# Kernel tuning notes

Measured on AMD Instinct MI355X. Metric: run time of the kernel, lower is better.

Reference implementation:

```python
import jax, jax.numpy as jnp
import numpy as np

D_MODEL = 768
N_LAYER = 4
VOCAB = 10000
N_MELS = 80
D_STATE = 16
D_CONV = 4
DT_RANK = 48          # ceil(768/16)
D_INNER = 1536        # expand * d_model
B_SZ, L_SEQ = 2, 1024


def rmsnorm(x, w, eps=1e-5):
    return x * jax.lax.rsqrt(jnp.mean(x * x, axis=-1, keepdims=True) + eps) * w


def causal_depthwise_conv(x, w, b):
    # x: (b, l, d_inner); w: (d_inner, 1, d_conv); torch Conv1d with padding=d_conv-1, truncated to l
    xc = jax.lax.conv_general_dilated(
        jnp.transpose(x, (0, 2, 1)), w, window_strides=(1,),
        padding=[(D_CONV - 1, 0)], dimension_numbers=('NCH', 'OIH', 'NCH'),
        feature_group_count=D_INNER)
    xc = xc + b[None, :, None]
    return jnp.transpose(xc, (0, 2, 1))


def selective_scan(u, dt, A, B, C, D):
    # u, dt: (b,l,d_in); A: (d_in,n); B,C: (b,l,n); D: (d_in,)
    dA = jnp.einsum('bld,dn->bldn', dt, A)
    dB_u = jnp.einsum('bld,bld,bln->bldn', dt, u, B)
    dA = jnp.clip(dA, -20, None)
    # shift dA by one step (exclusive cumulative decay), cumsum mode
    dA_shift = jnp.pad(dA[:, 1:], ((0, 0), (1, 0), (0, 0), (0, 0)))
    dA_cumsum = jnp.exp(jnp.cumsum(dA_shift, axis=1))
    x = jnp.cumsum(dB_u / (dA_cumsum + 1e-12), axis=1) * dA_cumsum
    y = jnp.einsum('bldn,bln->bld', x, C)
    return y + u * D


def mamba_block(x, rms_w, in_w, cw, cb, xp_w, dt_w, dt_b, A_log, Dp, out_w):
    h = rmsnorm(x, rms_w)
    xz = h @ in_w                       # (b,l,2*d_inner)
    xi, res = jnp.split(xz, 2, axis=-1)
    xi = jax.nn.silu(causal_depthwise_conv(xi, cw, cb))
    A = -jnp.exp(A_log.astype(jnp.float32))
    x_dbl = xi @ xp_w                   # (b,l,dt_rank+2n)
    delta = x_dbl[..., :DT_RANK]
    Bm = x_dbl[..., DT_RANK:DT_RANK + D_STATE]
    Cm = x_dbl[..., DT_RANK + D_STATE:]
    delta = jax.nn.softplus(delta @ dt_w + dt_b)
    y = selective_scan(xi, delta, A, Bm, Cm, Dp.astype(jnp.float32))
    y = y * jax.nn.silu(res)
    return y @ out_w + x


def setup_inputs():
    key = jax.random.key(0)
    ks = jax.random.split(key, 8)
    s = 0.02
    return {
        'input_ids': jax.random.randint(ks[0], (B_SZ, L_SEQ), 0, VOCAB),
        'embedding': jax.random.normal(ks[1], (VOCAB, D_MODEL), jnp.float32) * s,
        'rms_w': jnp.ones((N_LAYER, D_MODEL), jnp.float32),
        'in_proj_w': jax.random.normal(ks[2], (N_LAYER, D_MODEL, 2 * D_INNER), jnp.float32) * s,
        'conv_w': jax.random.normal(ks[3], (N_LAYER, D_INNER, 1, D_CONV), jnp.float32) * 0.1,
        'conv_b': jnp.zeros((N_LAYER, D_INNER), jnp.float32),
        'x_proj_w': jax.random.normal(ks[4], (N_LAYER, D_INNER, DT_RANK + 2 * D_STATE), jnp.float32) * s,
        'dt_proj_w': jax.random.normal(ks[5], (N_LAYER, DT_RANK, D_INNER), jnp.float32) * s,
        'dt_proj_b': jnp.zeros((N_LAYER, D_INNER), jnp.float32),
        'A_log': jnp.broadcast_to(jnp.log(jnp.arange(1, D_STATE + 1, dtype=jnp.float32)), (N_LAYER, D_INNER, D_STATE)) + 0.0,
        'D_param': jnp.ones((N_LAYER, D_INNER), jnp.float32),
        'out_proj_w': jax.random.normal(ks[6], (N_LAYER, D_INNER, D_MODEL), jnp.float32) * s,
        'norm_f_w': jnp.ones((D_MODEL,), jnp.float32),
        'head_w': jax.random.normal(ks[7], (D_MODEL, N_MELS), jnp.float32) * s,
    }


def reference(input_ids, embedding, rms_w, in_proj_w, conv_w, conv_b, x_proj_w,
              dt_proj_w, dt_proj_b, A_log, D_param, out_proj_w, norm_f_w, head_w):
    x = embedding[input_ids]            # (b,l,d)
    for i in range(N_LAYER):
        x = mamba_block(x, rms_w[i], in_proj_w[i], conv_w[i], conv_b[i],
                        x_proj_w[i], dt_proj_w[i], dt_proj_b[i], A_log[i],
                        D_param[i], out_proj_w[i])
    x = rmsnorm(x, norm_f_w)
    return x @ head_w                   # (b,l,n_mels)
```

## Files before the change

kernel.cpp:

```cpp
#include <hip/hip_runtime.h>
#include <hip/hip_bf16.h>
#include <math.h>

#define D_MODEL 768
#define N_LAYER 4
#define D_STATE 16
#define D_CONV  4
#define DT_RANK 48
#define D_INNER 1536
#define B_SZ    2
#define L_SEQ   1024
#define N_MELS  80
#define ROWS    (B_SZ * L_SEQ)

typedef __bf16 bf16x8 __attribute__((ext_vector_type(8)));
typedef unsigned short u16x8 __attribute__((ext_vector_type(8)));
typedef float  f32x4  __attribute__((ext_vector_type(4)));

__device__ __forceinline__ float fast_exp2(float x) {
    float r; asm("v_exp_f32 %0, %1" : "=v"(r) : "v"(x)); return r;
}
__device__ __forceinline__ float fast_exp(float x) {
    return fast_exp2(x * 1.44269504f);
}
__device__ __forceinline__ float fast_rcp(float x) {
    float r; asm("v_rcp_f32 %0, %1" : "=v"(r) : "v"(x)); return r;
}
__device__ __forceinline__ float silu_f(float v) {
    return v * fast_rcp(1.0f + fast_exp(-v));
}
__device__ __forceinline__ float softplus_f(float v) {
    return fmaxf(v, 0.0f) + log1pf(expf(-fabsf(v)));
}
__device__ __forceinline__ unsigned short f2bf(float f) {
    unsigned int u = __float_as_uint(f);
    unsigned int r = (u + 0x7FFFu + ((u >> 16) & 1u)) >> 16;
    return (unsigned short)r;
}
__device__ __forceinline__ float bf2f(unsigned short v) {
    return __uint_as_float(((unsigned int)v) << 16);
}

__global__ void embed_head_kernel(const int* __restrict__ ids,
                                  const float* __restrict__ emb,
                                  float* __restrict__ x,
                                  const float* __restrict__ head_w,
                                  unsigned short* __restrict__ headT) {
    int i = blockIdx.x * 256 + threadIdx.x;
    if (i < ROWS * D_MODEL) {
        int r = i / D_MODEL, c = i - r * D_MODEL;
        x[i] = emb[(size_t)ids[r] * D_MODEL + c];
    } else {
        int j = i - ROWS * D_MODEL;
        if (j < N_MELS * D_MODEL) {
            int c = j / D_MODEL, r = j - c * D_MODEL;
            headT[j] = f2bf(head_w[(size_t)r * N_MELS + c]);
        }
    }
}

__global__ void rmsnorm_kernel(const float* __restrict__ x,
                               const float* __restrict__ w,
                               unsigned short* __restrict__ hb) {
    int row = blockIdx.x;
    const float* xr = x + (size_t)row * D_MODEL;
    int tid = threadIdx.x;
    float p = 0.f;
    for (int c = tid; c < D_MODEL; c += 256) { float v = xr[c]; p = fmaf(v, v, p); }
    for (int off = 32; off >= 1; off >>= 1) p += __shfl_down(p, off, 64);
    __shared__ float ws[4];
    int lane = tid & 63, wv = tid >> 6;
    if (lane == 0) ws[wv] = p;
    __syncthreads();
    if (tid == 0) ws[0] = ws[0] + ws[1] + ws[2] + ws[3];
    __syncthreads();
    float scale = 1.0f / sqrtf(ws[0] / (float)D_MODEL + 1e-5f);
    for (int c = tid; c < D_MODEL; c += 256)
        hb[(size_t)row * D_MODEL + c] = f2bf(xr[c] * scale * w[c]);
}

__global__ void prep_weights_kernel(const float* __restrict__ in_wi,
                                    const float* __restrict__ out_wi,
                                    const float* __restrict__ xp_wi,
                                    const float* __restrict__ dt_wi,
                                    unsigned short* __restrict__ wt_in,
                                    unsigned short* __restrict__ wt_out,
                                    unsigned short* __restrict__ xpT,
                                    unsigned short* __restrict__ dtwT) {
    __shared__ float t[32][33];
    int bx = blockIdx.x;
    int tid = threadIdx.x;
    if (bx < 3456) {
        const float* src; unsigned short* dst; int R, C, cy, cx;
        if (bx < 2304) {
            src = in_wi; dst = wt_in; R = D_MODEL; C = 2 * D_INNER;
            cy = bx / 96; cx = bx - cy * 96;
        } else {
            int tt = bx - 2304;
            src = out_wi; dst = wt_out; R = D_INNER; C = D_MODEL;
            cy = tt / 24; cx = tt - cy * 24;
        }
        int tx = tid & 31, ty = tid >> 5;
        int r0 = cy * 32, c0 = cx * 32;
#pragma unroll
        for (int i = 0; i < 4; i++)
            t[ty + i * 8][tx] = src[(size_t)(r0 + ty + i * 8) * C + c0 + tx];
        __syncthreads();
#pragma unroll
        for (int i = 0; i < 4; i++)
            dst[(size_t)(c0 + ty + i * 8) * R + r0 + tx] = f2bf(t[tx][ty + i * 8]);
    } else {
        int i = (bx - 3456) * 256 + tid;
        if (i < 80 * D_INNER) {
            int c = i / D_INNER, r = i - c * D_INNER;
            xpT[i] = f2bf(xp_wi[(size_t)r * 80 + c]);
        } else {
            int i2 = i - 80 * D_INNER;
            int c = i2 >> 6, r = i2 & 63;
            dtwT[i2] = (r < DT_RANK) ? f2bf(dt_wi[(size_t)r * D_INNER + c])
                                     : (unsigned short)0;
        }
    }
}

__global__ void reduce_cvt_kernel(const float* __restrict__ part,
                                  float* __restrict__ xdbl,
                                  unsigned short* __restrict__ xdblb,
                                  int nsplit) {
    int i = blockIdx.x * 256 + threadIdx.x;
    if (i >= ROWS * 80) return;
    float s = 0.f;
    for (int k = 0; k < nsplit; k++) s += part[(size_t)k * ROWS * 80 + i];
    xdbl[i] = s;
    int r = i / 80, c = i - r * 80;
    if (c < DT_RANK) xdblb[r * 64 + c] = f2bf(s);
    else if (c >= 64) xdblb[r * 64 + c - 16] = 0;
}

__global__ void reduce_split_kernel(const float* __restrict__ part,
                                    float* __restrict__ dst,
                                    int MN, int nsplit) {
    int i = blockIdx.x * 256 + threadIdx.x;
    if (i >= MN) return;
    float s = 0.f;
    for (int k = 0; k < nsplit; k++) s += part[(size_t)k * MN + i];
    dst[i] = s;
}

__global__ __launch_bounds__(256) void mfma_gemm64(
        const unsigned short* __restrict__ A,
        const unsigned short* __restrict__ BT,
        const float* __restrict__ bias, const float* __restrict__ resid,
        float* __restrict__ Cf, unsigned short* __restrict__ Cb,
        int M, int N, int K, int ldc, int act, int bias_mode) {
    __shared__ unsigned short As[64][72];
    __shared__ unsigned short Bs[128][72];
    int tid = threadIdx.x;
    int row0 = blockIdx.y * 64, col0 = blockIdx.x * 128;
    int wave = tid >> 6, lane = tid & 63;
    int wr = (wave >> 1) * 32, wc = (wave & 1) * 64;
    int lm = lane & 15, lq = lane >> 4;
    int sr = tid >> 3, seg = tid & 7;
    const unsigned short* Ap0 = A  + (size_t)(row0 + sr) * K + seg * 8;
    const unsigned short* Ap1 = A  + (size_t)(row0 + 32 + sr) * K + seg * 8;
    const unsigned short* Bp0 = BT + (size_t)(col0 + sr) * K + seg * 8;
    const unsigned short* Bp1 = BT + (size_t)(col0 + 32 + sr) * K + seg * 8;
    const unsigned short* Bp2 = BT + (size_t)(col0 + 64 + sr) * K + seg * 8;
    const unsigned short* Bp3 = BT + (size_t)(col0 + 96 + sr) * K + seg * 8;
    f32x4 acc[2][4] = {};
    bf16x8 pa0 = *(const bf16x8*)Ap0;
    bf16x8 pa1 = *(const bf16x8*)Ap1;
    bf16x8 pb0 = *(const bf16x8*)Bp0;
    bf16x8 pb1 = *(const bf16x8*)Bp1;
    bf16x8 pb2 = *(const bf16x8*)Bp2;
    bf16x8 pb3 = *(const bf16x8*)Bp3;
    *(bf16x8*)&As[sr][seg * 8]      = pa0;
    *(bf16x8*)&As[32 + sr][seg * 8] = pa1;
    *(bf16x8*)&Bs[sr][seg * 8]      = pb0;
    *(bf16x8*)&Bs[32 + sr][seg * 8] = pb1;
    *(bf16x8*)&Bs[64 + sr][seg * 8] = pb2;
    *(bf16x8*)&Bs[96 + sr][seg * 8] = pb3;
    for (int k0 = 0; k0 < K; k0 += 64) {
        __syncthreads();
        bool more = (k0 + 64 < K);
        if (more) {
            pa0 = *(const bf16x8*)(Ap0 + k0 + 64);
            pa1 = *(const bf16x8*)(Ap1 + k0 + 64);
            pb0 = *(const bf16x8*)(Bp0 + k0 + 64);
            pb1 = *(const bf16x8*)(Bp1 + k0 + 64);
            pb2 = *(const bf16x8*)(Bp2 + k0 + 64);
            pb3 = *(const bf16x8*)(Bp3 + k0 + 64);
        }
#pragma unroll
        for (int ks = 0; ks < 2; ks++) {
            bf16x8 af[2], bfr[4];
#pragma unroll
            for (int i = 0; i < 2; i++)
                af[i] = *(const bf16x8*)&As[wr + i * 16 + lm][ks * 32 + lq * 8];
#pragma unroll
            for (int j = 0; j < 4; j++)
                bfr[j] = *(const bf16x8*)&Bs[wc + j * 16 + lm][ks * 32 + lq * 8];
#pragma unroll
            for (int i = 0; i < 2; i++)
#pragma unroll
                for (int j = 0; j < 4; j++)
                    acc[i][j] = __builtin_amdgcn_mfma_f32_16x16x32_bf16(af[i], bfr[j], acc[i][j], 0, 0, 0);
        }
        __syncthreads();
        if (more) {
            *(bf16x8*)&As[sr][seg * 8]      = pa0;
            *(bf16x8*)&As[32 + sr][seg * 8] = pa1;
            *(bf16x8*)&Bs[sr][seg * 8]      = pb0;
            *(bf16x8*)&Bs[32 + sr][seg * 8] = pb1;
            *(bf16x8*)&Bs[64 + sr][seg * 8] = pb2;
            *(bf16x8*)&Bs[96 + sr][seg * 8] = pb3;
        }
    }
#pragma unroll
    for (int i = 0; i < 2; i++) {
#pragma unroll
        for (int ii = 0; ii < 4; ii++) {
            int row = row0 + wr + i * 16 + lq * 4 + ii;
#pragma unroll
            for (int j = 0; j < 4; j++) {
                int col = col0 + wc + j * 16 + lm;
                float v = acc[i][j][ii];
                if (bias) v += bias[bias_mode ? row : col];
                if (act == 1) v = softplus_f(v);
                if (resid) v += resid[(size_t)row * ldc + col];
                if (Cf) Cf[(size_t)row * ldc + col] = v;
                else    Cb[(size_t)row * ldc + col] = f2bf(v);
            }
        }
    }
}

template<bool AT>
__global__ __launch_bounds__(256) void mfma_gemm32(
        const unsigned short* __restrict__ A,
        const unsigned short* __restrict__ BT,
        const float* __restrict__ bias, const float* __restrict__ resid,
        float* __restrict__ Cf, unsigned short* __restrict__ Cb,
        int M, int N, int K, int ldc, int act, int bias_mode) {
    __shared__ unsigned short As[32][72];
    __shared__ unsigned short Bs[128][72];
    int tid = threadIdx.x;
    int row0 = blockIdx.y * 32, col0 = blockIdx.x * 128;
    int wave = tid >> 6, lane = tid & 63;
    int wc = wave * 32;
    int lm = lane & 15, lq = lane >> 4;
    int sr = tid >> 3, seg = tid & 7;
    const unsigned short* Bp0 = BT + (size_t)(col0 + sr) * K + seg * 8;
    const unsigned short* Bp1 = BT + (size_t)(col0 + 32 + sr) * K + seg * 8;
    const unsigned short* Bp2 = BT + (size_t)(col0 + 64 + sr) * K + seg * 8;
    const unsigned short* Bp3 = BT + (size_t)(col0 + 96 + sr) * K + seg * 8;
    int akk = tid >> 2, arc = (tid & 3) * 8;
    const unsigned short* ApT = AT ? (A + (size_t)akk * M + row0 + arc) : nullptr;
    const unsigned short* Ap  = AT ? nullptr : (A + (size_t)(row0 + sr) * K + seg * 8);
    f32x4 acc[2][2] = {};
    u16x8 pa;
    if (AT) pa = *(const u16x8*)ApT;
    else    pa = *(const u16x8*)Ap;
    bf16x8 pb0 = *(const bf16x8*)Bp0;
    bf16x8 pb1 = *(const bf16x8*)Bp1;
    bf16x8 pb2 = *(const bf16x8*)Bp2;
    bf16x8 pb3 = *(const bf16x8*)Bp3;
    if (AT) {
#pragma unroll
        for (int j = 0; j < 8; j++) As[arc + j][akk] = pa[j];
    } else {
        *(u16x8*)&As[sr][seg * 8] = pa;
    }
    *(bf16x8*)&Bs[sr][seg * 8]      = pb0;
    *(bf16x8*)&Bs[32 + sr][seg * 8] = pb1;
    *(bf16x8*)&Bs[64 + sr][seg * 8] = pb2;
    *(bf16x8*)&Bs[96 + sr][seg * 8] = pb3;
    for (int k0 = 0; k0 < K; k0 += 64) {
        __syncthreads();
        bool more = (k0 + 64 < K);
        if (more) {
            if (AT) pa = *(const u16x8*)(ApT + (size_t)(k0 + 64) * M);
            else    pa = *(const u16x8*)(Ap + k0 + 64);
            pb0 = *(const bf16x8*)(Bp0 + k0 + 64);
            pb1 = *(const bf16x8*)(Bp1 + k0 + 64);
            pb2 = *(const bf16x8*)(Bp2 + k0 + 64);
            pb3 = *(const bf16x8*)(Bp3 + k0 + 64);
        }
#pragma unroll
        for (int ks = 0; ks < 2; ks++) {
            bf16x8 af[2], bfr[2];
#pragma unroll
            for (int i = 0; i < 2; i++)
                af[i] = *(const bf16x8*)&As[i * 16 + lm][ks * 32 + lq * 8];
#pragma unroll
            for (int j = 0; j < 2; j++)
                bfr[j] = *(const bf16x8*)&Bs[wc + j * 16 + lm][ks * 32 + lq * 8];
#pragma unroll
            for (int i = 0; i < 2; i++)
#pragma unroll
                for (int j = 0; j < 2; j++)
                    acc[i][j] = __builtin_amdgcn_mfma_f32_16x16x32_bf16(af[i], bfr[j], acc[i][j], 0, 0, 0);
        }
        __syncthreads();
        if (more) {
            if (AT) {
#pragma unroll
                for (int j = 0; j < 8; j++) As[arc + j][akk] = pa[j];
            } else {
                *(u16x8*)&As[sr][seg * 8] = pa;
            }
            *(bf16x8*)&Bs[sr][seg * 8]      = pb0;
            *(bf16x8*)&Bs[32 + sr][seg * 8] = pb1;
            *(bf16x8*)&Bs[64 + sr][seg * 8] = pb2;
            *(bf16x8*)&Bs[96 + sr][seg * 8] = pb3;
        }
    }
#pragma unroll
    for (int i = 0; i < 2; i++) {
#pragma unroll
        for (int ii = 0; ii < 4; ii++) {
            int row = row0 + i * 16 + lq * 4 + ii;
#pragma unroll
            for (int j = 0; j < 2; j++) {
                int col = col0 + wc + j * 16 + lm;
                float v = acc[i][j][ii];
                if (bias) v += bias[bias_mode ? row : col];
                if (act == 1) v = softplus_f(v);
                if (resid) v += resid[(size_t)row * ldc + col];
                if (Cf) Cf[(size_t)row * ldc + col] = v;
                else    Cb[(size_t)row * ldc + col] = f2bf(v);
            }
        }
    }
}

template<bool AT>
__global__ __launch_bounds__(256) void mfma_skinny(
        const unsigned short* __restrict__ A,
        const float* __restrict__ AfT,
        const unsigned short* __restrict__ BT,
        float* __restrict__ part,
        int M, int K, int kchunk) {
    constexpr int N = 80, NT = 5;
    __shared__ unsigned short As[128][40];
    __shared__ unsigned short Bs[80][40];
    int tid = threadIdx.x;
    int row0 = blockIdx.x * 128;
    int kb = blockIdx.y * kchunk, ke = kb + kchunk;
    float* myout = part + (size_t)blockIdx.y * M * N;
    int wave = tid >> 6, lane = tid & 63;
    int wr = wave * 32;
    int lm = lane & 15, lq = lane >> 4;
    int ar0 = tid >> 2, ar1 = (tid + 256) >> 2, aseg = tid & 3;
    const unsigned short* Ap0 = AT ? nullptr : (A + (size_t)(row0 + ar0) * K + aseg * 8);
    const unsigned short* Ap1 = AT ? nullptr : (A + (size_t)(row0 + ar1) * K + aseg * 8);
    int srl = tid >> 5, src4 = (tid & 31) * 4;
    const float* Af0 = AT ? (AfT + (size_t)(srl + 0) * M + row0 + src4) : nullptr;
    const float* Af1 = AT ? (AfT + (size_t)(srl + 8) * M + row0 + src4) : nullptr;
    const float* Af2 = AT ? (AfT + (size_t)(srl + 16) * M + row0 + src4) : nullptr;
    const float* Af3 = AT ? (AfT + (size_t)(srl + 24) * M + row0 + src4) : nullptr;
    const unsigned short* Bp0 = BT + (size_t)ar0 * K + aseg * 8;
    const unsigned short* Bp1 = BT + (size_t)ar1 * K + aseg * 8;
    bool haveB1 = (tid < 64);
    f32x4 acc[2][NT] = {};
    bf16x8 pa0, pa1;
    f32x4 qa0, qa1, qa2, qa3;
    if (AT) {
        qa0 = *(const f32x4*)(Af0 + (size_t)kb * M);
        qa1 = *(const f32x4*)(Af1 + (size_t)kb * M);
        qa2 = *(const f32x4*)(Af2 + (size_t)kb * M);
        qa3 = *(const f32x4*)(Af3 + (size_t)kb * M);
    } else {
        pa0 = *(const bf16x8*)(Ap0 + kb);
        pa1 = *(const bf16x8*)(Ap1 + kb);
    }
    bf16x8 pb0 = *(const bf16x8*)(Bp0 + kb);
    bf16x8 pb1 = {};
    if (haveB1) pb1 = *(const bf16x8*)(Bp1 + kb);
    if (AT) {
#pragma unroll
        for (int e = 0; e < 4; e++) {
            As[src4 + e][srl]      = f2bf(qa0[e]);
            As[src4 + e][srl + 8]  = f2bf(qa1[e]);
            As[src4 + e][srl + 16] = f2bf(qa2[e]);
            As[src4 + e][srl + 24] = f2bf(qa3[e]);
        }
    } else {
        *(bf16x8*)&As[ar0][aseg * 8] = pa0;
        *(bf16x8*)&As[ar1][aseg * 8] = pa1;
    }
    *(bf16x8*)&Bs[ar0][aseg * 8] = pb0;
    if (haveB1) *(bf16x8*)&Bs[ar1][aseg * 8] = pb1;
    for (int k0 = kb; k0 < ke; k0 += 32) {
        __syncthreads();
        bool more = (k0 + 32 < ke);
        if (more) {
            if (AT) {
                qa0 = *(const f32x4*)(Af0 + (size_t)(k0 + 32) * M);
                qa1 = *(const f32x4*)(Af1 + (size_t)(k0 + 32) * M);
                qa2 = *(const f32x4*)(Af2 + (size_t)(k0 + 32) * M);
                qa3 = *(const f32x4*)(Af3 + (size_t)(k0 + 32) * M);
            } else {
                pa0 = *(const bf16x8*)(Ap0 + k0 + 32);
                pa1 = *(const bf16x8*)(Ap1 + k0 + 32);
            }
            pb0 = *(const bf16x8*)(Bp0 + k0 + 32);
            if (haveB1) pb1 = *(const bf16x8*)(Bp1 + k0 + 32);
        }
        bf16x8 af[2], bfr[NT];
#pragma unroll
        for (int i = 0; i < 2; i++) af[i] = *(const bf16x8*)&As[wr + i * 16 + lm][lq * 8];
#pragma unroll
        for (int j = 0; j < NT; j++) bfr[j] = *(const bf16x8*)&Bs[j * 16 + lm][lq * 8];
#pragma unroll
        for (int i = 0; i < 2; i++)
#pragma unroll
            for (int j = 0; j < NT; j++)
                acc[i][j] = __builtin_amdgcn_mfma_f32_16x16x32_bf16(af[i], bfr[j], acc[i][j], 0, 0, 0);
        __syncthreads();
        if (more) {
            if (AT) {
#pragma unroll
                for (int e = 0; e < 4; e++) {
                    As[src4 + e][srl]      = f2bf(qa0[e]);
                    As[src4 + e][srl + 8]  = f2bf(qa1[e]);
                    As[src4 + e][srl + 16] = f2bf(qa2[e]);
                    As[src4 + e][srl + 24] = f2bf(qa3[e]);
                }
            } else {
                *(bf16x8*)&As[ar0][aseg * 8] = pa0;
                *(bf16x8*)&As[ar1][aseg * 8] = pa1;
            }
            *(bf16x8*)&Bs[ar0][aseg * 8] = pb0;
            if (haveB1) *(bf16x8*)&Bs[ar1][aseg * 8] = pb1;
        }
    }
#pragma unroll
    for (int i = 0; i < 2; i++) {
#pragma unroll
        for (int ii = 0; ii < 4; ii++) {
            int row = row0 + wr + i * 16 + lq * 4 + ii;
#pragma unroll
            for (int j = 0; j < NT; j++) {
                int col = j * 16 + lm;
                myout[(size_t)row * N + col] = acc[i][j][ii];
            }
        }
    }
}

__global__ __launch_bounds__(256) void conv_silu_kernel(
        const unsigned short* __restrict__ xzb,
        const float* __restrict__ cw,
        const float* __restrict__ cb,
        float* __restrict__ uT,
        unsigned short* __restrict__ resT) {
    __shared__ unsigned short s_xz[67][66];
    __shared__ float us[64][65];
    int tid = threadIdx.x;
    int d0 = blockIdx.x * 64, r0 = blockIdx.y * 64;
    bool atStart = (r0 & (L_SEQ - 1)) == 0;
    for (int idx = tid; idx < 67 * 64; idx += 256) {
        int rr = idx >> 6, cc2 = idx & 63;
        unsigned short v = 0;
        if (rr >= 3 || !atStart)
            v = xzb[(size_t)(r0 - 3 + rr) * (2 * D_INNER) + d0 + cc2];
        s_xz[rr][cc2] = v;
    }
    __syncthreads();
    int cc = tid & 63, ty = tid >> 6;
    const float* wp = cw + (size_t)(d0 + cc) * D_CONV;
    float w0 = wp[0], w1 = wp[1], w2 = wp[2], w3 = wp[3];
    float bb = cb[d0 + cc];
    for (int rr = ty; rr < 64; rr += 4) {
        float s = bb;
        s = fmaf(bf2f(s_xz[rr + 0][cc]), w0, s);
        s = fmaf(bf2f(s_xz[rr + 1][cc]), w1, s);
        s = fmaf(bf2f(s_xz[rr + 2][cc]), w2, s);
        s = fmaf(bf2f(s_xz[rr + 3][cc]), w3, s);
        us[rr][cc] = silu_f(s);
    }
    __syncthreads();
    int tx = tid & 63, dy = tid >> 6;
    for (int dd = dy; dd < 64; dd += 4)
        uT[(size_t)(d0 + dd) * ROWS + r0 + tx] = us[tx][dd];
    __syncthreads();
    for (int idx = tid; idx < 64 * 64; idx += 256) {
        int rr = idx >> 6, cc2 = idx & 63;
        s_xz[rr][cc2] = xzb[(size_t)(r0 + rr) * (2 * D_INNER) + D_INNER + d0 + cc2];
    }
    __syncthreads();
    for (int dd = dy; dd < 64; dd += 4)
        resT[(size_t)(d0 + dd) * ROWS + r0 + tx] = s_xz[tx][dd];
}

__global__ __launch_bounds__(256) void scan_kernel(
        const float* __restrict__ deltaT,
        const float* __restrict__ uT,
        const float* __restrict__ xdbl,
        const unsigned short* __restrict__ resT,
        const float* __restrict__ A_log,
        const float* __restrict__ Dp,
        unsigned short* __restrict__ ygT) {
    int tid = threadIdx.x;
    int n = tid & 15, c = tid >> 4;
    int bd = blockIdx.x;
    int b = bd / D_INNER, d = bd - b * D_INNER;
    int row0 = b * L_SEQ;
    float a2 = -fast_exp(A_log[d * D_STATE + n]) * 1.44269504f;
    float Dd = Dp[d];
    __shared__ float2 s_du[L_SEQ + 16];
    __shared__ float cs1[16][17];
    __shared__ float cs2[16][17];
    __shared__ float gmv[16];
    const float* dptr = deltaT + (size_t)d * ROWS + row0;
    const float* uptr = uT + (size_t)d * ROWS + row0;
    for (int e = tid; e < L_SEQ; e += 256)
        s_du[e + (e >> 6)] = make_float2(dptr[e], uptr[e]);
    __syncthreads();
    {
        int l0 = c * 64, sb = l0 + c;
        bool notfirst = (c != 0);
        float sum = 0.f;
#pragma unroll 8
        for (int j = 0; j < 64; j++) {
            float dA = fmaxf(s_du[sb + j].x * a2, -28.8539008f);
            if (j > 0 || notfirst) sum += dA;
        }
        cs1[n][c] = sum;
    }
    __syncthreads();
    float cbase = 0.f;
    for (int cc = 0; cc < c; cc++) cbase += cs1[n][cc];
    float gm = cbase;
    gm = fmaxf(gm, __shfl_xor(gm, 1, 16));
    gm = fmaxf(gm, __shfl_xor(gm, 2, 16));
    gm = fmaxf(gm, __shfl_xor(gm, 4, 16));
    gm = fmaxf(gm, __shfl_xor(gm, 8, 16));
    if (n == 0) gmv[c] = gm;
    __syncthreads();
    int lc = 16;
    for (int cc = 1; cc < 16; cc++)
        if (gmv[cc] <= -150.0f) { lc = cc; break; }
    int clen = lc * 4;
    int l0b = c * clen;
    int lend = lc * 64;
    {
        float sum = 0.f;
        for (int j = 0; j < clen; j++) {
            int l = l0b + j;
            float dA = fmaxf(s_du[l + (l >> 6)].x * a2, -28.8539008f);
            if (l > 0) sum += dA;
        }
        cs1[n][c] = sum;
    }
    __syncthreads();
    float cbase_b = 0.f;
    for (int cc = 0; cc < c; cc++) cbase_b += cs1[n][cc];
    const float* xBbase = xdbl + (size_t)row0 * 80 + DT_RANK + n;
    {
        float Cacc = cbase_b, psum = 0.f;
        for (int j = 0; j < clen; j++) {
            int l = l0b + j;
            float2 du = s_du[l + (l >> 6)];
            float dA = fmaxf(du.x * a2, -28.8539008f);
            if (l > 0) Cacc += dA;
            float S = fast_exp2(Cacc);
            float r = fast_rcp(S + 1e-12f);
            psum = fmaf(du.x * du.y * xBbase[l * 80], r, psum);
        }
        cs2[n][c] = psum;
    }
    __syncthreads();
    float pbase = 0.f;
    for (int cc = 0; cc < c; cc++) pbase += cs2[n][cc];
    {
        float Cacc = cbase_b, P = pbase;
        for (int j = 0; j < clen; j++) {
            int l = l0b + j;
            float2 du = s_du[l + (l >> 6)];
            float dA = fmaxf(du.x * a2, -28.8539008f);
            if (l > 0) Cacc += dA;
            float S = fast_exp2(Cacc);
            float r = fast_rcp(S + 1e-12f);
            P = fmaf(du.x * du.y * xBbase[l * 80], r, P);
            float contrib = P * S * xBbase[l * 80 + 16];
            contrib += __shfl_xor(contrib, 1, 16);
            contrib += __shfl_xor(contrib, 2, 16);
            contrib += __shfl_xor(contrib, 4, 16);
            contrib += __shfl_xor(contrib, 8, 16);
            if (n == 0) s_du[l + (l >> 6)].x = contrib + du.y * Dd;
        }
    }
    __syncthreads();
    const unsigned short* rptr = resT + (size_t)d * ROWS + row0;
    unsigned short* yout = ygT + (size_t)d * ROWS + row0;
    for (int e = tid; e < L_SEQ; e += 256) {
        float2 v = s_du[e + (e >> 6)];
        float y = (e < lend) ? v.x : v.y * Dd;
        float res = bf2f(rptr[e]);
        yout[e] = f2bf(y * silu_f(res));
    }
}

extern "C" void kernel_launch(void* const* d_in, const int* in_sizes, int n_in,
                              void* d_out, int out_size, void* d_ws, size_t ws_size,
                              hipStream_t stream) {
    const int*   ids    = (const int*)d_in[0];
    const float* emb    = (const float*)d_in[1];
    const float* rms_w  = (const float*)d_in[2];
    const float* in_w   = (const float*)d_in[3];
    const float* conv_w = (const float*)d_in[4];
    const float* conv_b = (const float*)d_in[5];
    const float* xp_w   = (const float*)d_in[6];
    const float* dt_w   = (const float*)d_in[7];
    const float* dt_b   = (const float*)d_in[8];
    const float* A_log  = (const float*)d_in[9];
    const float* Dp     = (const float*)d_in[10];
    const float* out_w  = (const float*)d_in[11];
    const float* nf_w   = (const float*)d_in[12];
    const float* head_w = (const float*)d_in[13];
    float* out = (float*)d_out;

    char* base = (char*)d_ws;
    float*          x      = (float*)(base + 0);
    unsigned short* hb     = (unsigned short*)(base + 6291456);
    unsigned short* xzb    = (unsigned short*)(base + 9437184);
    unsigned short* ygT    = (unsigned short*)(base + 9437184);
    float*          uT     = (float*)(base + 22020096);
    float*          xdbl   = (float*)(base + 40894464);
    unsigned short* xdblb  = (unsigned short*)(base + 41549824);
    float*          deltaT = (float*)(base + 41811968);
    float*          part   = (float*)(base + 41811968);
    unsigned short* resT   = (unsigned short*)(base + 54394880);
    unsigned short* wt_in  = (unsigned short*)(base + 60686336);
    unsigned short* wt_out = (unsigned short*)(base + 65404928);
    unsigned short* xpT    = (unsigned short*)(base + 67764224);
    unsigned short* dtwT   = (unsigned short*)(base + 68009984);
    unsigned short* headT  = (unsigned short*)(base + 68206592);

    embed_head_kernel<<<(ROWS * D_MODEL + N_MELS * D_MODEL + 255) / 256, 256, 0, stream>>>(
        ids, emb, x, head_w, headT);

    for (int i = 0; i < N_LAYER; i++) {
        const float* in_wi   = in_w + (size_t)i * D_MODEL * 2 * D_INNER;
        const float* conv_wi = conv_w + (size_t)i * D_INNER * D_CONV;
        const float* conv_bi = conv_b + (size_t)i * D_INNER;
        const float* xp_wi   = xp_w + (size_t)i * D_INNER * (DT_RANK + 2 * D_STATE);
        const float* dt_wi   = dt_w + (size_t)i * DT_RANK * D_INNER;
        const float* dt_bi   = dt_b + (size_t)i * D_INNER;
        const float* A_li    = A_log + (size_t)i * D_INNER * D_STATE;
        const float* Dpi     = Dp + (size_t)i * D_INNER;
        const float* out_wi  = out_w + (size_t)i * D_INNER * D_MODEL;
        const float* rms_wi  = rms_w + (size_t)i * D_MODEL;

        prep_weights_kernel<<<4320, 256, 0, stream>>>(
            in_wi, out_wi, xp_wi, dt_wi, wt_in, wt_out, xpT, dtwT);

        rmsnorm_kernel<<<ROWS, 256, 0, stream>>>(x, rms_wi, hb);
        mfma_gemm64<<<dim3(2 * D_INNER / 128, ROWS / 64), 256, 0, stream>>>(
            hb, wt_in, nullptr, nullptr, nullptr, xzb,
            ROWS, 2 * D_INNER, D_MODEL, 2 * D_INNER, 0, 0);
        conv_silu_kernel<<<dim3(D_INNER / 64, ROWS / 64), 256, 0, stream>>>(
            xzb, conv_wi, conv_bi, uT, resT);
        mfma_skinny<true><<<dim3(ROWS / 128, 16), 256, 0, stream>>>(
            nullptr, uT, xpT, part, ROWS, D_INNER, D_INNER / 16);
        reduce_cvt_kernel<<<(ROWS * 80 + 255) / 256, 256, 0, stream>>>(
            part, xdbl, xdblb, 16);
        mfma_gemm32<false><<<dim3(ROWS / 128, D_INNER / 32), 256, 0, stream>>>(
            dtwT, xdblb, dt_bi, nullptr, deltaT, nullptr,
            D_INNER, ROWS, 64, ROWS, 1, 1);
        scan_kernel<<<B_SZ * D_INNER, 256, 0, stream>>>(
            deltaT, uT, xdbl, resT, A_li, Dpi, ygT);
        mfma_gemm32<true><<<dim3(D_MODEL / 128, ROWS / 32), 256, 0, stream>>>(
            ygT, wt_out, nullptr, x, x, nullptr,
            ROWS, D_MODEL, D_INNER, D_MODEL, 0, 0);
    }

    rmsnorm_kernel<<<ROWS, 256, 0, stream>>>(x, nf_w, hb);
    mfma_skinny<false><<<dim3(ROWS / 128, 8), 256, 0, stream>>>(
        hb, nullptr, headT, part, ROWS, D_MODEL, D_MODEL / 8);
    reduce_split_kernel<<<(ROWS * N_MELS + 255) / 256, 256, 0, stream>>>(
        part, out, ROWS * N_MELS, 8);
}
```

Measured before the change: 681.3 us.

## Fuse dt projection and softplus into the scan kernel, specialize GEMM epilogues

The separate dt-projection GEMM, which wrote a float delta tensor, is removed. Each scan block now computes delta for its channel as a 48-wide bf16 dot product of the x_dbl row with that channel's dt weights, applies softplus, and writes the result straight into shared memory. This drops one kernel launch and the write and read of a D_INNER x ROWS float tensor. In exchange, every scan block rereads the x_dbl rows, which are shared across all channels, and does redundant scalar FMAs. The GEMM kernels also have their runtime-flag epilogues replaced by specialized fixed paths.

```diff
diff --git a/kernel.cpp b/kernel.cpp
--- a/kernel.cpp
+++ b/kernel.cpp
@@ -150,9 +150,8 @@
 __global__ __launch_bounds__(256) void mfma_gemm64(
         const unsigned short* __restrict__ A,
         const unsigned short* __restrict__ BT,
-        const float* __restrict__ bias, const float* __restrict__ resid,
-        float* __restrict__ Cf, unsigned short* __restrict__ Cb,
-        int M, int N, int K, int ldc, int act, int bias_mode) {
+        unsigned short* __restrict__ Cb,
+        int M, int N, int K, int ldc) {
     __shared__ unsigned short As[64][72];
     __shared__ unsigned short Bs[128][72];
     int tid = threadIdx.x;
@@ -224,24 +223,17 @@
 #pragma unroll
             for (int j = 0; j < 4; j++) {
                 int col = col0 + wc + j * 16 + lm;
-                float v = acc[i][j][ii];
-                if (bias) v += bias[bias_mode ? row : col];
-                if (act == 1) v = softplus_f(v);
-                if (resid) v += resid[(size_t)row * ldc + col];
-                if (Cf) Cf[(size_t)row * ldc + col] = v;
-                else    Cb[(size_t)row * ldc + col] = f2bf(v);
+                Cb[(size_t)row * ldc + col] = f2bf(acc[i][j][ii]);
             }
         }
     }
 }
 
-template<bool AT>
-__global__ __launch_bounds__(256) void mfma_gemm32(
-        const unsigned short* __restrict__ A,
+__global__ __launch_bounds__(256) void mfma_gemm32o(
+        const unsigned short* __restrict__ AT_,
         const unsigned short* __restrict__ BT,
-        const float* __restrict__ bias, const float* __restrict__ resid,
-        float* __restrict__ Cf, unsigned short* __restrict__ Cb,
-        int M, int N, int K, int ldc, int act, int bias_mode) {
+        const float* __restrict__ resid, float* __restrict__ Cf,
+        int M, int K, int ldc) {
     __shared__ unsigned short As[32][72];
     __shared__ unsigned short Bs[128][72];
     int tid = threadIdx.x;
@@ -255,22 +247,15 @@
     const unsigned short* Bp2 = BT + (size_t)(col0 + 64 + sr) * K + seg * 8;
     const unsigned short* Bp3 = BT + (size_t)(col0 + 96 + sr) * K + seg * 8;
     int akk = tid >> 2, arc = (tid & 3) * 8;
-    const unsigned short* ApT = AT ? (A + (size_t)akk * M + row0 + arc) : nullptr;
-    const unsigned short* Ap  = AT ? nullptr : (A + (size_t)(row0 + sr) * K + seg * 8);
+    const unsigned short* ApT = AT_ + (size_t)akk * M + row0 + arc;
     f32x4 acc[2][2] = {};
-    u16x8 pa;
-    if (AT) pa = *(const u16x8*)ApT;
-    else    pa = *(const u16x8*)Ap;
+    u16x8 pa = *(const u16x8*)ApT;
     bf16x8 pb0 = *(const bf16x8*)Bp0;
     bf16x8 pb1 = *(const bf16x8*)Bp1;
     bf16x8 pb2 = *(const bf16x8*)Bp2;
     bf16x8 pb3 = *(const bf16x8*)Bp3;
-    if (AT) {
-#pragma unroll
-        for (int j = 0; j < 8; j++) As[arc + j][akk] = pa[j];
-    } else {
-        *(u16x8*)&As[sr][seg * 8] = pa;
-    }
+#pragma unroll
+    for (int j = 0; j < 8; j++) As[arc + j][akk] = pa[j];
     *(bf16x8*)&Bs[sr][seg * 8]      = pb0;
     *(bf16x8*)&Bs[32 + sr][seg * 8] = pb1;
     *(bf16x8*)&Bs[64 + sr][seg * 8] = pb2;
@@ -279,8 +264,7 @@
         __syncthreads();
         bool more = (k0 + 64 < K);
         if (more) {
-            if (AT) pa = *(const u16x8*)(ApT + (size_t)(k0 + 64) * M);
-            else    pa = *(const u16x8*)(Ap + k0 + 64);
+            pa  = *(const u16x8*)(ApT + (size_t)(k0 + 64) * M);
             pb0 = *(const bf16x8*)(Bp0 + k0 + 64);
             pb1 = *(const bf16x8*)(Bp1 + k0 + 64);
             pb2 = *(const bf16x8*)(Bp2 + k0 + 64);
@@ -303,12 +287,8 @@
         }
         __syncthreads();
         if (more) {
-            if (AT) {
-#pragma unroll
-                for (int j = 0; j < 8; j++) As[arc + j][akk] = pa[j];
-            } else {
-                *(u16x8*)&As[sr][seg * 8] = pa;
-            }
+#pragma unroll
+            for (int j = 0; j < 8; j++) As[arc + j][akk] = pa[j];
             *(bf16x8*)&Bs[sr][seg * 8]      = pb0;
             *(bf16x8*)&Bs[32 + sr][seg * 8] = pb1;
             *(bf16x8*)&Bs[64 + sr][seg * 8] = pb2;
@@ -323,12 +303,7 @@
 #pragma unroll
             for (int j = 0; j < 2; j++) {
                 int col = col0 + wc + j * 16 + lm;
-                float v = acc[i][j][ii];
-                if (bias) v += bias[bias_mode ? row : col];
-                if (act == 1) v = softplus_f(v);
-                if (resid) v += resid[(size_t)row * ldc + col];
-                if (Cf) Cf[(size_t)row * ldc + col] = v;
-                else    Cb[(size_t)row * ldc + col] = f2bf(v);
+                Cf[(size_t)row * ldc + col] = acc[i][j][ii] + resid[(size_t)row * ldc + col];
             }
         }
     }
@@ -495,7 +470,9 @@
 }
 
 __global__ __launch_bounds__(256) void scan_kernel(
-        const float* __restrict__ deltaT,
+        const unsigned short* __restrict__ xdblb,
+        const unsigned short* __restrict__ dtwT,
+        const float* __restrict__ dt_b,
         const float* __restrict__ uT,
         const float* __restrict__ xdbl,
         const unsigned short* __restrict__ resT,
@@ -513,10 +490,38 @@
     __shared__ float cs1[16][17];
     __shared__ float cs2[16][17];
     __shared__ float gmv[16];
-    const float* dptr = deltaT + (size_t)d * ROWS + row0;
+    const unsigned short* dtw = dtwT + (size_t)d * 64;
+    u16x8 w0 = *(const u16x8*)(dtw);
+    u16x8 w1 = *(const u16x8*)(dtw + 8);
+    u16x8 w2 = *(const u16x8*)(dtw + 16);
+    u16x8 w3 = *(const u16x8*)(dtw + 24);
+    u16x8 w4 = *(const u16x8*)(dtw + 32);
+    u16x8 w5 = *(const u16x8*)(dtw + 40);
+    float dbias = dt_b[d];
     const float* uptr = uT + (size_t)d * ROWS + row0;
-    for (int e = tid; e < L_SEQ; e += 256)
-        s_du[e + (e >> 6)] = make_float2(dptr[e], uptr[e]);
+    for (int e = tid; e < L_SEQ; e += 256) {
+        const unsigned short* xr = xdblb + (size_t)(row0 + e) * 64;
+        u16x8 x0 = *(const u16x8*)(xr);
+        u16x8 x1 = *(const u16x8*)(xr + 8);
+        u16x8 x2 = *(const u16x8*)(xr + 16);
+        u16x8 x3 = *(const u16x8*)(xr + 24);
+        u16x8 x4 = *(const u16x8*)(xr + 32);
+        u16x8 x5 = *(const u16x8*)(xr + 40);
+        float dot = 0.f;
+#pragma unroll
+        for (int j = 0; j < 8; j++) dot = fmaf(bf2f(x0[j]), bf2f(w0[j]), dot);
+#pragma unroll
+        for (int j = 0; j < 8; j++) dot = fmaf(bf2f(x1[j]), bf2f(w1[j]), dot);
+#pragma unroll
+        for (int j = 0; j < 8; j++) dot = fmaf(bf2f(x2[j]), bf2f(w2[j]), dot);
+#pragma unroll
+        for (int j = 0; j < 8; j++) dot = fmaf(bf2f(x3[j]), bf2f(w3[j]), dot);
+#pragma unroll
+        for (int j = 0; j < 8; j++) dot = fmaf(bf2f(x4[j]), bf2f(w4[j]), dot);
+#pragma unroll
+        for (int j = 0; j < 8; j++) dot = fmaf(bf2f(x5[j]), bf2f(w5[j]), dot);
+        s_du[e + (e >> 6)] = make_float2(softplus_f(dot + dbias), uptr[e]);
+    }
     __syncthreads();
     {
         int l0 = c * 64, sb = l0 + c;
@@ -630,7 +635,6 @@
     float*          uT     = (float*)(base + 22020096);
     float*          xdbl   = (float*)(base + 40894464);
     unsigned short* xdblb  = (unsigned short*)(base + 41549824);
-    float*          deltaT = (float*)(base + 41811968);
     float*          part   = (float*)(base + 41811968);
     unsigned short* resT   = (unsigned short*)(base + 54394880);
     unsigned short* wt_in  = (unsigned short*)(base + 60686336);
@@ -659,22 +663,17 @@
 
         rmsnorm_kernel<<<ROWS, 256, 0, stream>>>(x, rms_wi, hb);
         mfma_gemm64<<<dim3(2 * D_INNER / 128, ROWS / 64), 256, 0, stream>>>(
-            hb, wt_in, nullptr, nullptr, nullptr, xzb,
-            ROWS, 2 * D_INNER, D_MODEL, 2 * D_INNER, 0, 0);
+            hb, wt_in, xzb, ROWS, 2 * D_INNER, D_MODEL, 2 * D_INNER);
         conv_silu_kernel<<<dim3(D_INNER / 64, ROWS / 64), 256, 0, stream>>>(
             xzb, conv_wi, conv_bi, uT, resT);
         mfma_skinny<true><<<dim3(ROWS / 128, 16), 256, 0, stream>>>(
             nullptr, uT, xpT, part, ROWS, D_INNER, D_INNER / 16);
         reduce_cvt_kernel<<<(ROWS * 80 + 255) / 256, 256, 0, stream>>>(
             part, xdbl, xdblb, 16);
-        mfma_gemm32<false><<<dim3(ROWS / 128, D_INNER / 32), 256, 0, stream>>>(
-            dtwT, xdblb, dt_bi, nullptr, deltaT, nullptr,
-            D_INNER, ROWS, 64, ROWS, 1, 1);
         scan_kernel<<<B_SZ * D_INNER, 256, 0, stream>>>(
-            deltaT, uT, xdbl, resT, A_li, Dpi, ygT);
-        mfma_gemm32<true><<<dim3(D_MODEL / 128, ROWS / 32), 256, 0, stream>>>(
-            ygT, wt_out, nullptr, x, x, nullptr,
-            ROWS, D_MODEL, D_INNER, D_MODEL, 0, 0);
+            xdblb, dtwT, dt_bi, uT, xdbl, resT, A_li, Dpi, ygT);
+        mfma_gemm32o<<<dim3(D_MODEL / 128, ROWS / 32), 256, 0, stream>>>(
+            ygT, wt_out, x, x, ROWS, D_INNER, D_MODEL);
     }
 
     rmsnorm_kernel<<<ROWS, 256, 0, stream>>>(x, nf_w, hb);
```

Measured after the change: 665.4 us. 1.02x faster.
